# Performance work log

Measured on AMD Instinct MI355X. Metric: run time of the kernel, lower is better.

Reference implementation:

```python
import jax, jax.numpy as jnp
import numpy as np

IN_SIZE, DIM_K, DIM_V = 1024, 1024, 1024
N = 8192


def setup_inputs() -> dict:
    key = jax.random.key(0)
    ks = jax.random.split(key, 7)
    s = 1.0 / np.sqrt(IN_SIZE)
    return {
        "x": jax.random.normal(ks[0], (N, IN_SIZE), dtype=jnp.float32),
        "Wq": jax.random.uniform(ks[1], (DIM_K, IN_SIZE), jnp.float32, -s, s),
        "bq": jax.random.uniform(ks[2], (DIM_K,), jnp.float32, -s, s),
        "Wk": jax.random.uniform(ks[3], (DIM_K, IN_SIZE), jnp.float32, -s, s),
        "bk": jax.random.uniform(ks[4], (DIM_K,), jnp.float32, -s, s),
        "Wv": jax.random.uniform(ks[5], (DIM_V, IN_SIZE), jnp.float32, -s, s),
        "bv": jax.random.uniform(ks[6], (DIM_V,), jnp.float32, -s, s),
    }


def reference(x, Wq, bq, Wk, bk, Wv, bv):
    norm = 1.0 / np.sqrt(DIM_K)
    Q = x @ Wq.T + bq          # [N, dim_k]
    K = x @ Wk.T + bk          # [N, dim_k]
    V = x @ Wv.T + bv          # [N, dim_v]
    scores = (Q.T @ K) * norm  # [dim_k, dim_k]
    atten = jax.nn.softmax(scores, axis=0)  # softmax over rows (torch dim=0)
    return V @ atten           # [N, dim_k] (requires dim_v == dim_k)
```

## Files before the change

kernel.cpp:

```cpp
#include <hip/hip_runtime.h>
#include <hip/hip_bf16.h>
#include <stdint.h>

using bf16 = __hip_bfloat16;
typedef __attribute__((ext_vector_type(8))) short bf16x8;
typedef __attribute__((ext_vector_type(4))) float f32x4;

__device__ __forceinline__ void gload_lds16(const void* g, void* l) {
  __builtin_amdgcn_global_load_lds(
      (__attribute__((address_space(1))) void*)(g),
      (__attribute__((address_space(3))) void*)(l), 16, 0, 0);
}

__device__ __forceinline__ unsigned short bf16_bits(float f) {
  bf16 b = __float2bfloat16(f);
  return *reinterpret_cast<unsigned short*>(&b);
}

__device__ __forceinline__ float b2f(unsigned short u) {
  union { unsigned int i; float f; } x;
  x.i = ((unsigned int)u) << 16;
  return x.f;
}

__global__ __launch_bounds__(256) void pre_all(
    const float* __restrict__ x, const float* __restrict__ Wq,
    const float* __restrict__ Wk, const float* __restrict__ Wv,
    unsigned short* __restrict__ xb, unsigned short* __restrict__ xt,
    float* __restrict__ part, unsigned short* __restrict__ Wqx2,
    unsigned short* __restrict__ Wkext, unsigned short* __restrict__ Wvtb) {
  __shared__ unsigned short tile[64][79];
  __shared__ float cw[4][64];
  const int by = blockIdx.y;
  const int c0 = blockIdx.x * 64;
  const int tr = threadIdx.x >> 4;
  const int tc4 = (threadIdx.x & 15) * 4;

  if (by < 128) {
    const int r0 = by * 64;
    float ca0 = 0.f, ca1 = 0.f, ca2 = 0.f, ca3 = 0.f;
#pragma unroll
    for (int p = 0; p < 4; ++p) {
      const int r = p * 16 + tr;
      float4 f =
          *reinterpret_cast<const float4*>(x + (size_t)(r0 + r) * 1024 + c0 + tc4);
      unsigned short u0 = bf16_bits(f.x), u1 = bf16_bits(f.y);
      unsigned short u2 = bf16_bits(f.z), u3 = bf16_bits(f.w);
      ushort4 u = {u0, u1, u2, u3};
      *reinterpret_cast<ushort4*>(xb + (size_t)(r0 + r) * 1024 + c0 + tc4) = u;
      tile[r][tc4] = u0;
      tile[r][tc4 + 1] = u1;
      tile[r][tc4 + 2] = u2;
      tile[r][tc4 + 3] = u3;
      ca0 += f.x;
      ca1 += f.y;
      ca2 += f.z;
      ca3 += f.w;
    }
    ca0 += __shfl_xor(ca0, 16); ca0 += __shfl_xor(ca0, 32);
    ca1 += __shfl_xor(ca1, 16); ca1 += __shfl_xor(ca1, 32);
    ca2 += __shfl_xor(ca2, 16); ca2 += __shfl_xor(ca2, 32);
    ca3 += __shfl_xor(ca3, 16); ca3 += __shfl_xor(ca3, 32);
    const int lane = threadIdx.x & 63, wv = threadIdx.x >> 6;
    if (lane < 16) {
      cw[wv][lane * 4] = ca0;
      cw[wv][lane * 4 + 1] = ca1;
      cw[wv][lane * 4 + 2] = ca2;
      cw[wv][lane * 4 + 3] = ca3;
    }
    __syncthreads();
    if (threadIdx.x < 64) {
      float s = cw[0][threadIdx.x] + cw[1][threadIdx.x] + cw[2][threadIdx.x] +
                cw[3][threadIdx.x];
      part[(size_t)by * 1024 + c0 + threadIdx.x] = s;
    }
#pragma unroll
    for (int p = 0; p < 4; ++p) {
      const int c = p * 16 + tr;
      ushort4 u = {tile[tc4][c], tile[tc4 + 1][c], tile[tc4 + 2][c],
                   tile[tc4 + 3][c]};
      *reinterpret_cast<ushort4*>(xt + (size_t)(c0 + c) * 8192 + r0 + tc4) = u;
    }
  } else {
    const int w = by - 128;
    const int widx = w >> 4;
    const int r0 = (w & 15) * 64;
    if (widx < 2) {
      const float* W = (widx == 0) ? Wq : Wk;
      unsigned short* out = (widx == 0) ? Wqx2 : Wkext;
#pragma unroll
      for (int p = 0; p < 4; ++p) {
        const int r = r0 + p * 16 + tr;
        float4 f =
            *reinterpret_cast<const float4*>(W + (size_t)r * 1024 + c0 + tc4);
        ushort4 u = {bf16_bits(f.x), bf16_bits(f.y), bf16_bits(f.z),
                     bf16_bits(f.w)};
        *reinterpret_cast<ushort4*>(out + (size_t)r * 2048 + c0 + tc4) = u;
        *reinterpret_cast<ushort4*>(out + (size_t)r * 2048 + 1024 + c0 + tc4) = u;
      }
    } else {
#pragma unroll
      for (int p = 0; p < 4; ++p) {
        const int r = p * 16 + tr;
        float4 f = *reinterpret_cast<const float4*>(Wv + (size_t)(r0 + r) * 1024 +
                                                    c0 + tc4);
        tile[r][tc4] = bf16_bits(f.x);
        tile[r][tc4 + 1] = bf16_bits(f.y);
        tile[r][tc4 + 2] = bf16_bits(f.z);
        tile[r][tc4 + 3] = bf16_bits(f.w);
      }
      __syncthreads();
#pragma unroll
      for (int p = 0; p < 4; ++p) {
        const int c = p * 16 + tr;
        ushort4 u = {tile[tc4][c], tile[tc4 + 1][c], tile[tc4 + 2][c],
                     tile[tc4 + 3][c]};
        *reinterpret_cast<ushort4*>(Wvtb + (size_t)(c0 + c) * 1024 + r0 + tc4) = u;
      }
    }
  }
}

template <int BIAS_MODE, int OUT_BF16, int XCD_SWZ, int CONCAT>
__global__ __launch_bounds__(256, 2) void gemm_nt(
    const bf16* __restrict__ A, const bf16* __restrict__ B,
    const float* __restrict__ bias, void* __restrict__ Cout, int M, int N,
    int K, int kChunk, float scale) {
  __shared__ __align__(128) char lds[65536];
  const int tid = threadIdx.x;
  const int lane = tid & 63;
  const int wv = tid >> 6;
  const int wm = wv >> 1, wn = wv & 1;

  int mt, nt;
  if (XCD_SWZ) {
    int lin = blockIdx.y * gridDim.x + blockIdx.x;
    int cpx = (gridDim.x * gridDim.y) >> 3;
    int swz = (lin & 7) * cpx + (lin >> 3);
    nt = swz % gridDim.x;
    mt = swz / gridDim.x;
  } else {
    nt = blockIdx.x;
    mt = blockIdx.y;
  }
  const int m0 = mt * 128, n0 = nt * 128;
  const int kBegin = blockIdx.z * kChunk;

  const char* srcA[4];
  const char* srcB[4];
  int dstOff[4];
#pragma unroll
  for (int t = 0; t < 4; ++t) {
    int o = wv * 4096 + t * 1024 + lane * 16;
    int row = o >> 7;
    int gcb = (o & 127) ^ ((row & 7) << 4);
    srcA[t] = (const char*)A + ((size_t)(m0 + row) * K + kBegin) * 2 + gcb;
    srcB[t] = (const char*)B + ((size_t)(n0 + row) * K + kBegin) * 2 + gcb;
    dstOff[t] = wv * 4096 + t * 1024;
  }

  const int xorv = (lane & 7) << 4;
  const int rowOff = (lane & 15) * 128;
  const int colHi = (lane >> 4) << 4;

#pragma unroll
  for (int t = 0; t < 4; ++t) gload_lds16(srcA[t], lds + dstOff[t]);
#pragma unroll
  for (int t = 0; t < 4; ++t) gload_lds16(srcB[t], lds + 32768 + dstOff[t]);
#pragma unroll
  for (int t = 0; t < 4; ++t) {
    srcA[t] += 128;
    srcB[t] += 128;
  }
  __syncthreads();

  f32x4 acc[4][4] = {};
  const int nk = kChunk >> 6;
  int cur = 0;
  for (int kt = 0; kt < nk; ++kt) {
    if (kt + 1 < nk) {
      const int nb = (cur ^ 1) * 16384;
#pragma unroll
      for (int t = 0; t < 4; ++t) gload_lds16(srcA[t], lds + nb + dstOff[t]);
#pragma unroll
      for (int t = 0; t < 4; ++t)
        gload_lds16(srcB[t], lds + 32768 + nb + dstOff[t]);
#pragma unroll
      for (int t = 0; t < 4; ++t) {
        srcA[t] += 128;
        srcB[t] += 128;
      }
    }
    const char* baseA = lds + cur * 16384;
    const char* baseB = lds + 32768 + cur * 16384;
#pragma unroll
    for (int h = 0; h < 2; ++h) {
      const int kk64 = h * 64;
      bf16x8 af[4], bfr[4];
#pragma unroll
      for (int f = 0; f < 4; ++f)
        af[f] = *reinterpret_cast<const bf16x8*>(
            baseA + ((wm * 64 + f * 16) * 128) + rowOff + ((kk64 + colHi) ^ xorv));
#pragma unroll
      for (int f = 0; f < 4; ++f)
        bfr[f] = *reinterpret_cast<const bf16x8*>(
            baseB + ((wn * 64 + f * 16) * 128) + rowOff + ((kk64 + colHi) ^ xorv));
      __builtin_amdgcn_s_setprio(1);
#pragma unroll
      for (int m = 0; m < 4; ++m)
#pragma unroll
        for (int n = 0; n < 4; ++n)
          acc[m][n] = __builtin_amdgcn_mfma_f32_16x16x32_bf16(af[m], bfr[n],
                                                              acc[m][n], 0, 0, 0);
      __builtin_amdgcn_s_setprio(0);
    }
    __syncthreads();
    cur ^= 1;
  }

  const int ldC = CONCAT ? (int)(gridDim.z * N) : N;
  const int cOff = CONCAT ? (int)(blockIdx.z * N) : 0;
  char* Cbase = (char*)Cout;
  if (!CONCAT) Cbase += (size_t)blockIdx.z * M * N * (OUT_BF16 ? 2 : 4);
#pragma unroll
  for (int m = 0; m < 4; ++m) {
    const int grow = m0 + wm * 64 + m * 16 + ((lane >> 4) << 2);
#pragma unroll
    for (int n = 0; n < 4; ++n) {
      const int gcol = n0 + wn * 64 + n * 16 + (lane & 15);
#pragma unroll
      for (int r = 0; r < 4; ++r) {
        float v = acc[m][n][r] * scale;
        if (BIAS_MODE == 2) v += bias[gcol];
        if (OUT_BF16)
          ((bf16*)Cbase)[(size_t)(grow + r) * ldC + cOff + gcol] =
              __float2bfloat16(v);
        else
          ((float*)Cbase)[(size_t)(grow + r) * ldC + cOff + gcol] = v;
      }
    }
  }
}

template <int BIAS_MODE, int OUT_BF16, int XCD_SWZ, int CONCAT>
__global__ __launch_bounds__(256, 4) void gemm_nt64(
    const bf16* __restrict__ A, const bf16* __restrict__ B,
    const float* __restrict__ bias, void* __restrict__ Cout, int M, int N,
    int K, int kChunk, float scale) {
  __shared__ __align__(128) char lds[16384];
  const int tid = threadIdx.x;
  const int lane = tid & 63;
  const int wv = tid >> 6;
  const int wm = wv >> 1, wn = wv & 1;

  int mt, nt;
  if (XCD_SWZ) {
    int lin = blockIdx.y * gridDim.x + blockIdx.x;
    int cpx = (gridDim.x * gridDim.y) >> 3;
    int swz = (lin & 7) * cpx + (lin >> 3);
    nt = swz % gridDim.x;
    mt = swz / gridDim.x;
  } else {
    nt = blockIdx.x;
    mt = blockIdx.y;
  }
  const int m0 = mt * 64, n0 = nt * 64;
  const int kBegin = blockIdx.z * kChunk;

  const char* srcA[2];
  const char* srcB[2];
  int dstOff[2];
#pragma unroll
  for (int t = 0; t < 2; ++t) {
    int o = wv * 2048 + t * 1024 + lane * 16;
    int row = o >> 7;
    int gcb = (o & 127) ^ ((row & 7) << 4);
    srcA[t] = (const char*)A + ((size_t)(m0 + row) * K + kBegin) * 2 + gcb;
    srcB[t] = (const char*)B + ((size_t)(n0 + row) * K + kBegin) * 2 + gcb;
    dstOff[t] = wv * 2048 + t * 1024;
  }

  const int xorv = (lane & 7) << 4;
  const int rowOff = (lane & 15) * 128;
  const int colHi = (lane >> 4) << 4;

  f32x4 acc[2][2] = {};
  const int nk = kChunk >> 6;
  for (int kt = 0; kt < nk; ++kt) {
#pragma unroll
    for (int t = 0; t < 2; ++t) gload_lds16(srcA[t], lds + dstOff[t]);
#pragma unroll
    for (int t = 0; t < 2; ++t) gload_lds16(srcB[t], lds + 8192 + dstOff[t]);
#pragma unroll
    for (int t = 0; t < 2; ++t) {
      srcA[t] += 128;
      srcB[t] += 128;
    }
    __syncthreads();
#pragma unroll
    for (int h = 0; h < 2; ++h) {
      const int kk64 = h * 64;
      bf16x8 af[2], bfr[2];
#pragma unroll
      for (int f = 0; f < 2; ++f)
        af[f] = *reinterpret_cast<const bf16x8*>(
            lds + ((wm * 32 + f * 16) * 128) + rowOff + ((kk64 + colHi) ^ xorv));
#pragma unroll
      for (int f = 0; f < 2; ++f)
        bfr[f] = *reinterpret_cast<const bf16x8*>(
            lds + 8192 + ((wn * 32 + f * 16) * 128) + rowOff +
            ((kk64 + colHi) ^ xorv));
      __builtin_amdgcn_s_setprio(1);
#pragma unroll
      for (int m = 0; m < 2; ++m)
#pragma unroll
        for (int n = 0; n < 2; ++n)
          acc[m][n] = __builtin_amdgcn_mfma_f32_16x16x32_bf16(af[m], bfr[n],
                                                              acc[m][n], 0, 0, 0);
      __builtin_amdgcn_s_setprio(0);
    }
    __syncthreads();
  }

  const int ldC = CONCAT ? (int)(gridDim.z * N) : N;
  const int cOff = CONCAT ? (int)(blockIdx.z * N) : 0;
  char* Cbase = (char*)Cout;
  if (!CONCAT) Cbase += (size_t)blockIdx.z * M * N * (OUT_BF16 ? 2 : 4);
#pragma unroll
  for (int m = 0; m < 2; ++m) {
    const int grow = m0 + wm * 32 + m * 16 + ((lane >> 4) << 2);
#pragma unroll
    for (int n = 0; n < 2; ++n) {
      const int gcol = n0 + wn * 32 + n * 16 + (lane & 15);
#pragma unroll
      for (int r = 0; r < 4; ++r) {
        float v = acc[m][n][r] * scale;
        if (BIAS_MODE == 2) v += bias[gcol];
        if (OUT_BF16)
          ((bf16*)Cbase)[(size_t)(grow + r) * ldC + cOff + gcol] =
              __float2bfloat16(v);
        else
          ((float*)Cbase)[(size_t)(grow + r) * ldC + cOff + gcol] = v;
      }
    }
  }
}

__global__ __launch_bounds__(256) void gext_svuw(
    const float* __restrict__ Sp, unsigned short* __restrict__ Gext,
    const float* __restrict__ part, const float* __restrict__ Wq,
    const float* __restrict__ Wk, float* __restrict__ uw) {
  __shared__ float svl[1024];
  const int tid = threadIdx.x;
  if (blockIdx.x < 1024) {
    const int k = blockIdx.x;
    const int c4 = tid * 4;
    float g[4] = {0.f, 0.f, 0.f, 0.f};
#pragma unroll
    for (int z = 0; z < 8; ++z) {
      float4 f = *reinterpret_cast<const float4*>(Sp + ((size_t)z << 20) +
                                                  (size_t)k * 1024 + c4);
      g[0] += f.x;
      g[1] += f.y;
      g[2] += f.z;
      g[3] += f.w;
    }
    ushort4 hi, lo;
    unsigned short* h = &hi.x;
    unsigned short* l = &lo.x;
#pragma unroll
    for (int q = 0; q < 4; ++q) {
      unsigned short b = bf16_bits(g[q]);
      h[q] = b;
      l[q] = bf16_bits(g[q] - b2f(b));
    }
    *reinterpret_cast<ushort4*>(Gext + (size_t)k * 2048 + c4) = hi;
    *reinterpret_cast<ushort4*>(Gext + (size_t)k * 2048 + 1024 + c4) = lo;
  } else {
    float4 a = {0.f, 0.f, 0.f, 0.f};
    for (int p = 0; p < 128; ++p) {
      float4 f =
          *reinterpret_cast<const float4*>(part + (size_t)p * 1024 + tid * 4);
      a.x += f.x;
      a.y += f.y;
      a.z += f.z;
      a.w += f.w;
    }
    *reinterpret_cast<float4*>(svl + tid * 4) = a;
    __syncthreads();

    const int lane = tid & 63, wv = tid >> 6;
    const int lane16 = lane & 15, rsub = lane >> 4;
    const int row = (blockIdx.x - 1024) * 16 + wv * 4 + rsub;
    const float* W = (row < 1024) ? (Wq + (size_t)row * 1024)
                                  : (Wk + (size_t)(row - 1024) * 1024);
    float acc = 0.f;
#pragma unroll
    for (int q = 0; q < 16; ++q) {
      const int c = (lane16 + q * 16) * 4;
      float4 wv4 = *reinterpret_cast<const float4*>(W + c);
      float4 s4 = *reinterpret_cast<const float4*>(svl + c);
      acc += wv4.x * s4.x + wv4.y * s4.y + wv4.z * s4.z + wv4.w * s4.w;
    }
#pragma unroll
    for (int off = 1; off < 16; off <<= 1) acc += __shfl_xor(acc, off);
    if (lane16 == 0) uw[row] = acc;
  }
}

__global__ __launch_bounds__(256) void softmax_corr_r(
    const float* __restrict__ Stp, const float* __restrict__ uw,
    const float* __restrict__ bq, const float* __restrict__ bk,
    const float* __restrict__ bv, bf16* __restrict__ At,
    float* __restrict__ rv) {
  const int j = blockIdx.x;
  const int tid = threadIdx.x;
  const int lane = tid & 63, wv = tid >> 6;
  const float a1 = bk[j];
  const float a2 = uw[1024 + j] + 8192.0f * a1;
  const float norm = 0.03125f;
  float v[4];
#pragma unroll
  for (int t = 0; t < 4; ++t) {
    const int i = tid + 256 * t;
    float s = Stp[(size_t)j * 1024 + i] + Stp[(1ull << 20) + (size_t)j * 1024 + i];
    v[t] = norm * (s + a1 * uw[i] + a2 * bq[i]);
  }
  float m = fmaxf(fmaxf(v[0], v[1]), fmaxf(v[2], v[3]));
#pragma unroll
  for (int off = 32; off; off >>= 1) m = fmaxf(m, __shfl_xor(m, off));
  __shared__ float red[12];
  if (lane == 0) red[wv] = m;
  __syncthreads();
  m = fmaxf(fmaxf(red[0], red[1]), fmaxf(red[2], red[3]));
  float p[4], s = 0.f, pr = 0.f;
#pragma unroll
  for (int t = 0; t < 4; ++t) {
    p[t] = __expf(v[t] - m);
    s += p[t];
    pr += p[t] * bv[tid + 256 * t];
  }
#pragma unroll
  for (int off = 32; off; off >>= 1) {
    s += __shfl_xor(s, off);
    pr += __shfl_xor(pr, off);
  }
  if (lane == 0) {
    red[4 + wv] = s;
    red[8 + wv] = pr;
  }
  __syncthreads();
  const float inv = 1.f / (red[4] + red[5] + red[6] + red[7]);
#pragma unroll
  for (int t = 0; t < 4; ++t)
    At[(size_t)j * 1024 + tid + 256 * t] = __float2bfloat16(p[t] * inv);
  if (tid == 0) rv[j] = (red[8] + red[9] + red[10] + red[11]) * inv;
}

extern "C" void kernel_launch(void* const* d_in, const int* in_sizes, int n_in,
                              void* d_out, int out_size, void* d_ws,
                              size_t ws_size, hipStream_t stream) {
  const float* x = (const float*)d_in[0];
  const float* Wq = (const float*)d_in[1];
  const float* bq = (const float*)d_in[2];
  const float* Wk = (const float*)d_in[3];
  const float* bk = (const float*)d_in[4];
  const float* Wv = (const float*)d_in[5];
  const float* bv = (const float*)d_in[6];
  (void)in_sizes;
  (void)n_in;
  (void)out_size;
  (void)ws_size;

  char* ws = (char*)d_ws;
  const size_t MB = 1ull << 20;
  bf16* xb = (bf16*)(ws);
  bf16* xt = (bf16*)(ws + 16 * MB);
  float* SpG = (float*)(ws + 32 * MB);
  bf16* Wkext = (bf16*)(ws + 64 * MB);
  bf16* Wqx2 = (bf16*)(ws + 68 * MB);
  bf16* Wvtb = (bf16*)(ws + 72 * MB);
  bf16* Gext = (bf16*)(ws + 74 * MB);
  bf16* T1x = (bf16*)(ws + 78 * MB);
  float* Stp = (float*)(ws + 82 * MB);
  bf16* At = (bf16*)(ws + 90 * MB);
  bf16* Ftb = (bf16*)(ws + 92 * MB);
  float* uw = (float*)(ws + 94 * MB);
  float* rv = (float*)(ws + 94 * MB + 16384);
  float* part = (float*)(ws + 95 * MB);

  pre_all<<<dim3(16, 176), 256, 0, stream>>>(
      x, Wq, Wk, Wv, (unsigned short*)xb, (unsigned short*)xt, part,
      (unsigned short*)Wqx2, (unsigned short*)Wkext, (unsigned short*)Wvtb);
  gemm_nt<0, 0, 1, 0><<<dim3(8, 8, 8), 256, 0, stream>>>(
      xt, xt, nullptr, SpG, 1024, 1024, 8192, 1024, 1.0f);
  gext_svuw<<<1152, 256, 0, stream>>>(SpG, (unsigned short*)Gext, part, Wq, Wk,
                                      uw);
  gemm_nt64<0, 1, 1, 1><<<dim3(16, 16, 2), 256, 0, stream>>>(
      Wkext, Gext, nullptr, T1x, 1024, 1024, 2048, 1024, 1.0f);
  gemm_nt64<0, 0, 1, 0><<<dim3(16, 16, 2), 256, 0, stream>>>(
      T1x, Wqx2, nullptr, Stp, 1024, 1024, 2048, 1024, 1.0f);
  softmax_corr_r<<<1024, 256, 0, stream>>>(Stp, uw, bq, bk, bv, At, rv);
  gemm_nt64<0, 1, 1, 0><<<dim3(16, 16), 256, 0, stream>>>(
      At, Wvtb, nullptr, Ftb, 1024, 1024, 1024, 1024, 1.0f);
  gemm_nt<2, 0, 1, 0><<<dim3(8, 64), 256, 0, stream>>>(
      xb, Ftb, rv, d_out, 8192, 1024, 1024, 1024, 1.0f);
}
```

Before: 118.9 us.

## Exploit symmetry of Gram matrix x^T x by computing only lower-triangular tiles

The split-K Gram GEMM (xt·xtᵀ) now launches only the 36 lower-triangular 128x128 tile pairs per K-chunk (288 blocks instead of 512), using a triangular index decode. The reduction/split kernel then builds the full bf16 hi/lo Gram matrix by reading the computed tile and writing its transpose through an LDS tile for mirrored positions. This removes nearly half of the largest K=8192 GEMM's MFMA work, at the cost of a serial triangular index loop and a transpose pass in the reduction kernel.

Result: faster. 108.3 us (-8.9%).

```diff
diff --git a/kernel.cpp b/kernel.cpp
--- a/kernel.cpp
+++ b/kernel.cpp
@@ -121,12 +121,143 @@
   }
 }
 
-template <int BIAS_MODE, int OUT_BF16, int XCD_SWZ, int CONCAT>
+template <int BIAS_MODE, int OUT_BF16, int XCD_SWZ, int CONCAT, int TRI>
 __global__ __launch_bounds__(256, 2) void gemm_nt(
     const bf16* __restrict__ A, const bf16* __restrict__ B,
     const float* __restrict__ bias, void* __restrict__ Cout, int M, int N,
     int K, int kChunk, float scale) {
   __shared__ __align__(128) char lds[65536];
+  const int tid = threadIdx.x;
+  const int lane = tid & 63;
+  const int wv = tid >> 6;
+  const int wm = wv >> 1, wn = wv & 1;
+
+  int mt, nt, zz;
+  if (TRI) {
+    const int lin = blockIdx.x;
+    zz = lin & 7;
+    const int p = lin >> 3;
+    int ii = 0;
+    while ((ii + 1) * (ii + 2) / 2 <= p) ++ii;
+    mt = ii;
+    nt = p - ii * (ii + 1) / 2;
+  } else if (XCD_SWZ) {
+    int lin = blockIdx.y * gridDim.x + blockIdx.x;
+    int cpx = (gridDim.x * gridDim.y) >> 3;
+    int swz = (lin & 7) * cpx + (lin >> 3);
+    nt = swz % gridDim.x;
+    mt = swz / gridDim.x;
+    zz = blockIdx.z;
+  } else {
+    nt = blockIdx.x;
+    mt = blockIdx.y;
+    zz = blockIdx.z;
+  }
+  const int m0 = mt * 128, n0 = nt * 128;
+  const int kBegin = zz * kChunk;
+
+  const char* srcA[4];
+  const char* srcB[4];
+  int dstOff[4];
+#pragma unroll
+  for (int t = 0; t < 4; ++t) {
+    int o = wv * 4096 + t * 1024 + lane * 16;
+    int row = o >> 7;
+    int gcb = (o & 127) ^ ((row & 7) << 4);
+    srcA[t] = (const char*)A + ((size_t)(m0 + row) * K + kBegin) * 2 + gcb;
+    srcB[t] = (const char*)B + ((size_t)(n0 + row) * K + kBegin) * 2 + gcb;
+    dstOff[t] = wv * 4096 + t * 1024;
+  }
+
+  const int xorv = (lane & 7) << 4;
+  const int rowOff = (lane & 15) * 128;
+  const int colHi = (lane >> 4) << 4;
+
+#pragma unroll
+  for (int t = 0; t < 4; ++t) gload_lds16(srcA[t], lds + dstOff[t]);
+#pragma unroll
+  for (int t = 0; t < 4; ++t) gload_lds16(srcB[t], lds + 32768 + dstOff[t]);
+#pragma unroll
+  for (int t = 0; t < 4; ++t) {
+    srcA[t] += 128;
+    srcB[t] += 128;
+  }
+  __syncthreads();
+
+  f32x4 acc[4][4] = {};
+  const int nk = kChunk >> 6;
+  int cur = 0;
+  for (int kt = 0; kt < nk; ++kt) {
+    if (kt + 1 < nk) {
+      const int nb = (cur ^ 1) * 16384;
+#pragma unroll
+      for (int t = 0; t < 4; ++t) gload_lds16(srcA[t], lds + nb + dstOff[t]);
+#pragma unroll
+      for (int t = 0; t < 4; ++t)
+        gload_lds16(srcB[t], lds + 32768 + nb + dstOff[t]);
+#pragma unroll
+      for (int t = 0; t < 4; ++t) {
+        srcA[t] += 128;
+        srcB[t] += 128;
+      }
+    }
+    const char* baseA = lds + cur * 16384;
+    const char* baseB = lds + 32768 + cur * 16384;
+#pragma unroll
+    for (int h = 0; h < 2; ++h) {
+      const int kk64 = h * 64;
+      bf16x8 af[4], bfr[4];
+#pragma unroll
+      for (int f = 0; f < 4; ++f)
+        af[f] = *reinterpret_cast<const bf16x8*>(
+            baseA + ((wm * 64 + f * 16) * 128) + rowOff + ((kk64 + colHi) ^ xorv));
+#pragma unroll
+      for (int f = 0; f < 4; ++f)
+        bfr[f] = *reinterpret_cast<const bf16x8*>(
+            baseB + ((wn * 64 + f * 16) * 128) + rowOff + ((kk64 + colHi) ^ xorv));
+      __builtin_amdgcn_s_setprio(1);
+#pragma unroll
+      for (int m = 0; m < 4; ++m)
+#pragma unroll
+        for (int n = 0; n < 4; ++n)
+          acc[m][n] = __builtin_amdgcn_mfma_f32_16x16x32_bf16(af[m], bfr[n],
+                                                              acc[m][n], 0, 0, 0);
+      __builtin_amdgcn_s_setprio(0);
+    }
+    __syncthreads();
+    cur ^= 1;
+  }
+
+  const int ldC = CONCAT ? (int)(gridDim.z * N) : N;
+  const int cOff = CONCAT ? (int)(zz * N) : 0;
+  char* Cbase = (char*)Cout;
+  if (!CONCAT) Cbase += (size_t)zz * M * N * (OUT_BF16 ? 2 : 4);
+#pragma unroll
+  for (int m = 0; m < 4; ++m) {
+    const int grow = m0 + wm * 64 + m * 16 + ((lane >> 4) << 2);
+#pragma unroll
+    for (int n = 0; n < 4; ++n) {
+      const int gcol = n0 + wn * 64 + n * 16 + (lane & 15);
+#pragma unroll
+      for (int r = 0; r < 4; ++r) {
+        float v = acc[m][n][r] * scale;
+        if (BIAS_MODE == 2) v += bias[gcol];
+        if (OUT_BF16)
+          ((bf16*)Cbase)[(size_t)(grow + r) * ldC + cOff + gcol] =
+              __float2bfloat16(v);
+        else
+          ((float*)Cbase)[(size_t)(grow + r) * ldC + cOff + gcol] = v;
+      }
+    }
+  }
+}
+
+template <int BIAS_MODE, int OUT_BF16, int XCD_SWZ, int CONCAT>
+__global__ __launch_bounds__(256, 4) void gemm_nt64(
+    const bf16* __restrict__ A, const bf16* __restrict__ B,
+    const float* __restrict__ bias, void* __restrict__ Cout, int M, int N,
+    int K, int kChunk, float scale) {
+  __shared__ __align__(128) char lds[16384];
   const int tid = threadIdx.x;
   const int lane = tid & 63;
   const int wv = tid >> 6;
@@ -143,79 +274,62 @@
     nt = blockIdx.x;
     mt = blockIdx.y;
   }
-  const int m0 = mt * 128, n0 = nt * 128;
+  const int m0 = mt * 64, n0 = nt * 64;
   const int kBegin = blockIdx.z * kChunk;
 
-  const char* srcA[4];
-  const char* srcB[4];
-  int dstOff[4];
-#pragma unroll
-  for (int t = 0; t < 4; ++t) {
-    int o = wv * 4096 + t * 1024 + lane * 16;
+  const char* srcA[2];
+  const char* srcB[2];
+  int dstOff[2];
+#pragma unroll
+  for (int t = 0; t < 2; ++t) {
+    int o = wv * 2048 + t * 1024 + lane * 16;
     int row = o >> 7;
     int gcb = (o & 127) ^ ((row & 7) << 4);
     srcA[t] = (const char*)A + ((size_t)(m0 + row) * K + kBegin) * 2 + gcb;
     srcB[t] = (const char*)B + ((size_t)(n0 + row) * K + kBegin) * 2 + gcb;
-    dstOff[t] = wv * 4096 + t * 1024;
+    dstOff[t] = wv * 2048 + t * 1024;
   }
 
   const int xorv = (lane & 7) << 4;
   const int rowOff = (lane & 15) * 128;
   const int colHi = (lane >> 4) << 4;
 
-#pragma unroll
-  for (int t = 0; t < 4; ++t) gload_lds16(srcA[t], lds + dstOff[t]);
-#pragma unroll
-  for (int t = 0; t < 4; ++t) gload_lds16(srcB[t], lds + 32768 + dstOff[t]);
-#pragma unroll
-  for (int t = 0; t < 4; ++t) {
-    srcA[t] += 128;
-    srcB[t] += 128;
-  }
-  __syncthreads();
-
-  f32x4 acc[4][4] = {};
+  f32x4 acc[2][2] = {};
   const int nk = kChunk >> 6;
-  int cur = 0;
   for (int kt = 0; kt < nk; ++kt) {
-    if (kt + 1 < nk) {
-      const int nb = (cur ^ 1) * 16384;
-#pragma unroll
-      for (int t = 0; t < 4; ++t) gload_lds16(srcA[t], lds + nb + dstOff[t]);
-#pragma unroll
-      for (int t = 0; t < 4; ++t)
-        gload_lds16(srcB[t], lds + 32768 + nb + dstOff[t]);
-#pragma unroll
-      for (int t = 0; t < 4; ++t) {
-        srcA[t] += 128;
-        srcB[t] += 128;
-      }
-    }
-    const char* baseA = lds + cur * 16384;
-    const char* baseB = lds + 32768 + cur * 16384;
+#pragma unroll
+    for (int t = 0; t < 2; ++t) gload_lds16(srcA[t], lds + dstOff[t]);
+#pragma unroll
+    for (int t = 0; t < 2; ++t) gload_lds16(srcB[t], lds + 8192 + dstOff[t]);
+#pragma unroll
+    for (int t = 0; t < 2; ++t) {
+      srcA[t] += 128;
+      srcB[t] += 128;
+    }
+    __syncthreads();
 #pragma unroll
     for (int h = 0; h < 2; ++h) {
       const int kk64 = h * 64;
-      bf16x8 af[4], bfr[4];
-#pragma unroll
-      for (int f = 0; f < 4; ++f)
+      bf16x8 af[2], bfr[2];
+#pragma unroll
+      for (int f = 0; f < 2; ++f)
         af[f] = *reinterpret_cast<const bf16x8*>(
-            baseA + ((wm * 64 + f * 16) * 128) + rowOff + ((kk64 + colHi) ^ xorv));
-#pragma unroll
-      for (int f = 0; f < 4; ++f)
+            lds + ((wm * 32 + f * 16) * 128) + rowOff + ((kk64 + colHi) ^ xorv));
+#pragma unroll
+      for (int f = 0; f < 2; ++f)
         bfr[f] = *reinterpret_cast<const bf16x8*>(
-            baseB + ((wn * 64 + f * 16) * 128) + rowOff + ((kk64 + colHi) ^ xorv));
+            lds + 8192 + ((wn * 32 + f * 16) * 128) + rowOff +
+            ((kk64 + colHi) ^ xorv));
       __builtin_amdgcn_s_setprio(1);
 #pragma unroll
-      for (int m = 0; m < 4; ++m)
-#pragma unroll
-        for (int n = 0; n < 4; ++n)
+      for (int m = 0; m < 2; ++m)
+#pragma unroll
+        for (int n = 0; n < 2; ++n)
           acc[m][n] = __builtin_amdgcn_mfma_f32_16x16x32_bf16(af[m], bfr[n],
                                                               acc[m][n], 0, 0, 0);
       __builtin_amdgcn_s_setprio(0);
     }
     __syncthreads();
-    cur ^= 1;
   }
 
   const int ldC = CONCAT ? (int)(gridDim.z * N) : N;
@@ -223,11 +337,11 @@
   char* Cbase = (char*)Cout;
   if (!CONCAT) Cbase += (size_t)blockIdx.z * M * N * (OUT_BF16 ? 2 : 4);
 #pragma unroll
-  for (int m = 0; m < 4; ++m) {
-    const int grow = m0 + wm * 64 + m * 16 + ((lane >> 4) << 2);
-#pragma unroll
-    for (int n = 0; n < 4; ++n) {
-      const int gcol = n0 + wn * 64 + n * 16 + (lane & 15);
+  for (int m = 0; m < 2; ++m) {
+    const int grow = m0 + wm * 32 + m * 16 + ((lane >> 4) << 2);
+#pragma unroll
+    for (int n = 0; n < 2; ++n) {
+      const int gcol = n0 + wn * 32 + n * 16 + (lane & 15);
 #pragma unroll
       for (int r = 0; r < 4; ++r) {
         float v = acc[m][n][r] * scale;
@@ -242,140 +356,66 @@
   }
 }
 
-template <int BIAS_MODE, int OUT_BF16, int XCD_SWZ, int CONCAT>
-__global__ __launch_bounds__(256, 4) void gemm_nt64(
-    const bf16* __restrict__ A, const bf16* __restrict__ B,
-    const float* __restrict__ bias, void* __restrict__ Cout, int M, int N,
-    int K, int kChunk, float scale) {
-  __shared__ __align__(128) char lds[16384];
-  const int tid = threadIdx.x;
-  const int lane = tid & 63;
-  const int wv = tid >> 6;
-  const int wm = wv >> 1, wn = wv & 1;
-
-  int mt, nt;
-  if (XCD_SWZ) {
-    int lin = blockIdx.y * gridDim.x + blockIdx.x;
-    int cpx = (gridDim.x * gridDim.y) >> 3;
-    int swz = (lin & 7) * cpx + (lin >> 3);
-    nt = swz % gridDim.x;
-    mt = swz / gridDim.x;
-  } else {
-    nt = blockIdx.x;
-    mt = blockIdx.y;
-  }
-  const int m0 = mt * 64, n0 = nt * 64;
-  const int kBegin = blockIdx.z * kChunk;
-
-  const char* srcA[2];
-  const char* srcB[2];
-  int dstOff[2];
-#pragma unroll
-  for (int t = 0; t < 2; ++t) {
-    int o = wv * 2048 + t * 1024 + lane * 16;
-    int row = o >> 7;
-    int gcb = (o & 127) ^ ((row & 7) << 4);
-    srcA[t] = (const char*)A + ((size_t)(m0 + row) * K + kBegin) * 2 + gcb;
-    srcB[t] = (const char*)B + ((size_t)(n0 + row) * K + kBegin) * 2 + gcb;
-    dstOff[t] = wv * 2048 + t * 1024;
-  }
-
-  const int xorv = (lane & 7) << 4;
-  const int rowOff = (lane & 15) * 128;
-  const int colHi = (lane >> 4) << 4;
-
-  f32x4 acc[2][2] = {};
-  const int nk = kChunk >> 6;
-  for (int kt = 0; kt < nk; ++kt) {
-#pragma unroll
-    for (int t = 0; t < 2; ++t) gload_lds16(srcA[t], lds + dstOff[t]);
-#pragma unroll
-    for (int t = 0; t < 2; ++t) gload_lds16(srcB[t], lds + 8192 + dstOff[t]);
-#pragma unroll
-    for (int t = 0; t < 2; ++t) {
-      srcA[t] += 128;
-      srcB[t] += 128;
-    }
-    __syncthreads();
-#pragma unroll
-    for (int h = 0; h < 2; ++h) {
-      const int kk64 = h * 64;
-      bf16x8 af[2], bfr[2];
-#pragma unroll
-      for (int f = 0; f < 2; ++f)
-        af[f] = *reinterpret_cast<const bf16x8*>(
-            lds + ((wm * 32 + f * 16) * 128) + rowOff + ((kk64 + colHi) ^ xorv));
-#pragma unroll
-      for (int f = 0; f < 2; ++f)
-        bfr[f] = *reinterpret_cast<const bf16x8*>(
-            lds + 8192 + ((wn * 32 + f * 16) * 128) + rowOff +
-            ((kk64 + colHi) ^ xorv));
-      __builtin_amdgcn_s_setprio(1);
-#pragma unroll
-      for (int m = 0; m < 2; ++m)
-#pragma unroll
-        for (int n = 0; n < 2; ++n)
-          acc[m][n] = __builtin_amdgcn_mfma_f32_16x16x32_bf16(af[m], bfr[n],
-                                                              acc[m][n], 0, 0, 0);
-      __builtin_amdgcn_s_setprio(0);
-    }
-    __syncthreads();
-  }
-
-  const int ldC = CONCAT ? (int)(gridDim.z * N) : N;
-  const int cOff = CONCAT ? (int)(blockIdx.z * N) : 0;
-  char* Cbase = (char*)Cout;
-  if (!CONCAT) Cbase += (size_t)blockIdx.z * M * N * (OUT_BF16 ? 2 : 4);
-#pragma unroll
-  for (int m = 0; m < 2; ++m) {
-    const int grow = m0 + wm * 32 + m * 16 + ((lane >> 4) << 2);
-#pragma unroll
-    for (int n = 0; n < 2; ++n) {
-      const int gcol = n0 + wn * 32 + n * 16 + (lane & 15);
-#pragma unroll
-      for (int r = 0; r < 4; ++r) {
-        float v = acc[m][n][r] * scale;
-        if (BIAS_MODE == 2) v += bias[gcol];
-        if (OUT_BF16)
-          ((bf16*)Cbase)[(size_t)(grow + r) * ldC + cOff + gcol] =
-              __float2bfloat16(v);
-        else
-          ((float*)Cbase)[(size_t)(grow + r) * ldC + cOff + gcol] = v;
-      }
-    }
-  }
-}
-
 __global__ __launch_bounds__(256) void gext_svuw(
     const float* __restrict__ Sp, unsigned short* __restrict__ Gext,
     const float* __restrict__ part, const float* __restrict__ Wq,
     const float* __restrict__ Wk, float* __restrict__ uw) {
+  __shared__ float tf[64][65];
   __shared__ float svl[1024];
   const int tid = threadIdx.x;
-  if (blockIdx.x < 1024) {
-    const int k = blockIdx.x;
-    const int c4 = tid * 4;
-    float g[4] = {0.f, 0.f, 0.f, 0.f};
-#pragma unroll
-    for (int z = 0; z < 8; ++z) {
-      float4 f = *reinterpret_cast<const float4*>(Sp + ((size_t)z << 20) +
-                                                  (size_t)k * 1024 + c4);
-      g[0] += f.x;
-      g[1] += f.y;
-      g[2] += f.z;
-      g[3] += f.w;
-    }
-    ushort4 hi, lo;
-    unsigned short* h = &hi.x;
-    unsigned short* l = &lo.x;
-#pragma unroll
-    for (int q = 0; q < 4; ++q) {
-      unsigned short b = bf16_bits(g[q]);
-      h[q] = b;
-      l[q] = bf16_bits(g[q] - b2f(b));
-    }
-    *reinterpret_cast<ushort4*>(Gext + (size_t)k * 2048 + c4) = hi;
-    *reinterpret_cast<ushort4*>(Gext + (size_t)k * 2048 + 1024 + c4) = lo;
+  const int bx = blockIdx.x;
+  if (bx < 256) {
+    const int ti = bx >> 4, tj = bx & 15;
+    const bool mirror = (ti >> 1) < (tj >> 1);
+    const int si = mirror ? tj : ti, sj = mirror ? ti : tj;
+    const int r = tid >> 4, c4 = (tid & 15) * 4;
+#pragma unroll
+    for (int pass = 0; pass < 4; ++pass) {
+      const int row = pass * 16 + r;
+      float g0 = 0.f, g1 = 0.f, g2 = 0.f, g3 = 0.f;
+#pragma unroll
+      for (int z = 0; z < 8; ++z) {
+        float4 f = *reinterpret_cast<const float4*>(
+            Sp + ((size_t)z << 20) + (size_t)(si * 64 + row) * 1024 + sj * 64 + c4);
+        g0 += f.x;
+        g1 += f.y;
+        g2 += f.z;
+        g3 += f.w;
+      }
+      if (!mirror) {
+        ushort4 hi, lo;
+        unsigned short bb;
+        bb = bf16_bits(g0); hi.x = bb; lo.x = bf16_bits(g0 - b2f(bb));
+        bb = bf16_bits(g1); hi.y = bb; lo.y = bf16_bits(g1 - b2f(bb));
+        bb = bf16_bits(g2); hi.z = bb; lo.z = bf16_bits(g2 - b2f(bb));
+        bb = bf16_bits(g3); hi.w = bb; lo.w = bf16_bits(g3 - b2f(bb));
+        const size_t base = (size_t)(ti * 64 + row) * 2048 + tj * 64 + c4;
+        *reinterpret_cast<ushort4*>(Gext + base) = hi;
+        *reinterpret_cast<ushort4*>(Gext + base + 1024) = lo;
+      } else {
+        tf[row][c4] = g0;
+        tf[row][c4 + 1] = g1;
+        tf[row][c4 + 2] = g2;
+        tf[row][c4 + 3] = g3;
+      }
+    }
+    if (mirror) {
+      __syncthreads();
+#pragma unroll
+      for (int pass = 0; pass < 4; ++pass) {
+        const int crow = pass * 16 + r;
+        ushort4 hi, lo;
+        unsigned short bb;
+        float g;
+        g = tf[c4][crow];     bb = bf16_bits(g); hi.x = bb; lo.x = bf16_bits(g - b2f(bb));
+        g = tf[c4 + 1][crow]; bb = bf16_bits(g); hi.y = bb; lo.y = bf16_bits(g - b2f(bb));
+        g = tf[c4 + 2][crow]; bb = bf16_bits(g); hi.z = bb; lo.z = bf16_bits(g - b2f(bb));
+        g = tf[c4 + 3][crow]; bb = bf16_bits(g); hi.w = bb; lo.w = bf16_bits(g - b2f(bb));
+        const size_t base = (size_t)(ti * 64 + crow) * 2048 + tj * 64 + c4;
+        *reinterpret_cast<ushort4*>(Gext + base) = hi;
+        *reinterpret_cast<ushort4*>(Gext + base + 1024) = lo;
+      }
+    }
   } else {
     float4 a = {0.f, 0.f, 0.f, 0.f};
     for (int p = 0; p < 128; ++p) {
@@ -391,7 +431,7 @@
 
     const int lane = tid & 63, wv = tid >> 6;
     const int lane16 = lane & 15, rsub = lane >> 4;
-    const int row = (blockIdx.x - 1024) * 16 + wv * 4 + rsub;
+    const int row = (bx - 256) * 16 + wv * 4 + rsub;
     const float* W = (row < 1024) ? (Wq + (size_t)row * 1024)
                                   : (Wk + (size_t)(row - 1024) * 1024);
     float acc = 0.f;
@@ -492,10 +532,10 @@
   pre_all<<<dim3(16, 176), 256, 0, stream>>>(
       x, Wq, Wk, Wv, (unsigned short*)xb, (unsigned short*)xt, part,
       (unsigned short*)Wqx2, (unsigned short*)Wkext, (unsigned short*)Wvtb);
-  gemm_nt<0, 0, 1, 0><<<dim3(8, 8, 8), 256, 0, stream>>>(
+  gemm_nt<0, 0, 0, 0, 1><<<288, 256, 0, stream>>>(
       xt, xt, nullptr, SpG, 1024, 1024, 8192, 1024, 1.0f);
-  gext_svuw<<<1152, 256, 0, stream>>>(SpG, (unsigned short*)Gext, part, Wq, Wk,
-                                      uw);
+  gext_svuw<<<384, 256, 0, stream>>>(SpG, (unsigned short*)Gext, part, Wq, Wk,
+                                     uw);
   gemm_nt64<0, 1, 1, 1><<<dim3(16, 16, 2), 256, 0, stream>>>(
       Wkext, Gext, nullptr, T1x, 1024, 1024, 2048, 1024, 1.0f);
   gemm_nt64<0, 0, 1, 0><<<dim3(16, 16, 2), 256, 0, stream>>>(
@@ -503,6 +543,6 @@
   softmax_corr_r<<<1024, 256, 0, stream>>>(Stp, uw, bq, bk, bv, At, rv);
   gemm_nt64<0, 1, 1, 0><<<dim3(16, 16), 256, 0, stream>>>(
       At, Wvtb, nullptr, Ftb, 1024, 1024, 1024, 1024, 1.0f);
-  gemm_nt<2, 0, 1, 0><<<dim3(8, 64), 256, 0, stream>>>(
+  gemm_nt<2, 0, 1, 0, 0><<<dim3(8, 64), 256, 0, stream>>>(
       xb, Ftb, rv, d_out, 8192, 1024, 1024, 1024, 1.0f);
 }
```
